# Performance work log

Measured on AMD Instinct MI355X. Metric: run time of the kernel, lower is better.

The kernel has to match this reference:

```python
import jax, jax.numpy as jnp
import numpy as np

NUM_HEADS = 8
HEAD_SPLITS = (2, 3, 3)      # heads per CRPE window (CoaT default {3:2,5:3,7:3})
KERNELS = (3, 5, 7)
DIM = 256
CH = DIM // NUM_HEADS        # 32
N_DET = 100


def setup_inputs() -> dict:
    key = jax.random.key(0)
    ks = jax.random.split(key, 12)
    B, Hs, Ws, C = 4, 128, 128, DIM
    N = Hs * Ws
    inp = {
        "x": jax.random.normal(ks[0], (B, N, C), dtype=jnp.float32),
        "det": jax.random.normal(ks[1], (B, N_DET, C), dtype=jnp.float32),
        "H": Hs,
        "W": Ws,
        # qkv Linear (dim -> 3*dim, bias=True); stored as [in, out] for x @ W
        "qkv_w": jax.random.normal(ks[2], (C, 3 * C), dtype=jnp.float32) * 0.02,
        "qkv_b": jnp.zeros((3 * C,), dtype=jnp.float32),
        # output proj Linear (dim -> dim)
        "proj_w": jax.random.normal(ks[3], (C, C), dtype=jnp.float32) * 0.02,
        "proj_b": jnp.zeros((C,), dtype=jnp.float32),
    }
    # CRPE depthwise conv weights: per window k, channels = head_split * CH
    for i, (hs, k) in enumerate(zip(HEAD_SPLITS, KERNELS)):
        ch = hs * CH
        inp[f"crpe_w{k}"] = jax.random.normal(ks[4 + i], (ch, 1, k, k), dtype=jnp.float32) * 0.05
        inp[f"crpe_b{k}"] = jnp.zeros((ch,), dtype=jnp.float32)
    return inp


def _crpe(q, v, H, W, crpe_w3, crpe_b3, crpe_w5, crpe_b5, crpe_w7, crpe_b7):
    # q, v: [B, h, N, Ch], N == H*W  (CoaT ConvRelPosEnc)
    B, h, N, Ch = q.shape
    v_img = jnp.transpose(v, (0, 1, 3, 2)).reshape(B, h * Ch, H, W)
    splits = np.cumsum([hs * Ch for hs in HEAD_SPLITS])[:-1]
    parts = jnp.split(v_img, splits, axis=1)
    ws = (crpe_w3, crpe_w5, crpe_w7)
    bs = (crpe_b3, crpe_b5, crpe_b7)
    outs = []
    for part, w, b, k in zip(parts, ws, bs, KERNELS):
        pad = k // 2
        o = jax.lax.conv_general_dilated(
            part, w, window_strides=(1, 1), padding=[(pad, pad), (pad, pad)],
            feature_group_count=part.shape[1],  # depthwise
            dimension_numbers=("NCHW", "OIHW", "NCHW"))
        outs.append(o + b[None, :, None, None])
    conv_v = jnp.concatenate(outs, axis=1).reshape(B, h, Ch, N)
    conv_v = jnp.transpose(conv_v, (0, 1, 3, 2))  # [B,h,N,Ch]
    return q * conv_v


def reference(x, det, H, W, qkv_w, qkv_b, proj_w, proj_b,
              crpe_w3, crpe_b3, crpe_w5, crpe_b5, crpe_w7, crpe_b7):
    B, N, C = x.shape
    h = NUM_HEADS
    Ch = C // h
    scale = Ch ** (-0.5)

    xcat = jnp.concatenate([x, det], axis=1)          # [B, N+M, C]
    full_qkv = xcat @ qkv_w + qkv_b                   # [B, N+M, 3C]

    # ---- patch branch: factorized (linear) attention + CRPE ----
    patch_qkv = full_qkv[:, :N, :].reshape(B, N, 3, h, Ch)
    patch_qkv = jnp.transpose(patch_qkv, (2, 0, 3, 1, 4))  # [3,B,h,N,Ch]
    pq, pk, pv = patch_qkv[0], patch_qkv[1], patch_qkv[2]
    k_softmax = jax.nn.softmax(pk, axis=2)                 # softmax over tokens
    factor = jnp.einsum('bhnc,bhnd->bhcd', k_softmax, pv)  # [B,h,Ch,Ch]
    factor_att = jnp.einsum('bhnc,bhcd->bhnd', pq, factor) # [B,h,N,Ch]
    crpe = _crpe(pq, pv, H, W, crpe_w3, crpe_b3, crpe_w5, crpe_b5, crpe_w7, crpe_b7)
    patch_x = scale * factor_att + crpe
    patch_x = jnp.transpose(patch_x, (0, 2, 1, 3)).reshape(B, N, C)

    # ---- det branch: standard softmax self-attention ----
    det_qkv = full_qkv[:, N:, :].reshape(B, -1, 3, h, Ch)
    det_qkv = jnp.transpose(det_qkv, (2, 0, 3, 1, 4))      # [3,B,h,M,Ch]
    dq, dk, dv = det_qkv[0], det_qkv[1], det_qkv[2]
    attn = jax.nn.softmax((dq * scale) @ jnp.swapaxes(dk, -2, -1), axis=-1)
    det_x = jnp.transpose(attn @ dv, (0, 2, 1, 3)).reshape(B, -1, C)

    out = jnp.concatenate([patch_x, det_x], axis=1) @ proj_w + proj_b
    return out[:, :N, :], out[:, N:, :]
```

## Files before the change

### kernel.cpp

```cpp
#include <hip/hip_runtime.h>
#include <hip/hip_fp16.h>

#define NHEADS 8
#define CHD 32
#define CDIM 256
#define C3 768
#define NTOK 16384
#define MDET 100
#define TPB (NTOK + MDET)
#define BATCH 4
#define ROWS (BATCH * TPB)
#define HH 128
#define WW 128
#define SCALE 0.17677669529663687f
#define SCH 32
#define FCH 16

typedef unsigned short u16;
typedef __attribute__((ext_vector_type(8))) __bf16 bf16x8;
typedef __attribute__((ext_vector_type(4))) float f32x4;

__device__ __forceinline__ float bf2f(u16 u) {
  union { unsigned int i; float f; } z; z.i = ((unsigned int)u) << 16; return z.f;
}
__device__ __forceinline__ u16 f2bf(float f) {
  __bf16 h = (__bf16)f;
  return __builtin_bit_cast(unsigned short, h);
}

static const size_t B_QX     = 0;
static const size_t B_KPL    = B_QX + (size_t)ROWS * 256 * 2;
static const size_t B_VPL    = B_KPL + (size_t)ROWS * 256 * 2;
static const size_t B_WQT    = B_VPL + (size_t)ROWS * 256 * 2;
static const size_t B_WPT    = B_WQT + (size_t)768 * 256 * 2;
static const size_t B_PM     = B_WPT + (size_t)256 * 256 * 2;
static const size_t B_PS     = B_PM + 1024 * 32 * 4;
static const size_t B_FPART  = B_PS + 1024 * 32 * 4;
static const size_t B_FACTOR = B_FPART + (size_t)512 * 1024 * 4;
static const size_t B_LSE    = B_FACTOR + 32768 * 4;
static const size_t B_END    = B_LSE + 1024 * 4;

__global__ __launch_bounds__(256)
void wconv(const float* __restrict__ qkv_w, const float* __restrict__ proj_w,
           u16* __restrict__ WqT, u16* __restrict__ WpT) {
  int o = blockIdx.x * 256 + threadIdx.x;
  if (o < 768 * 256) {
    int n = o >> 8, k = o & 255;
    WqT[o] = f2bf(qkv_w[(size_t)k * C3 + n]);
  } else {
    int p = o - 768 * 256;
    int n = p >> 8, k = p & 255;
    WpT[p] = f2bf(proj_w[(size_t)k * CDIM + n]);
  }
}

__global__ __launch_bounds__(256)
void gemm_qkv(const float* __restrict__ x, const float* __restrict__ det,
              const u16* __restrict__ WqT, const float* __restrict__ bias,
              u16* __restrict__ qx, u16* __restrict__ kpl, __half* __restrict__ vpl) {
  const int row0 = blockIdx.x * 128;
  const int col0 = blockIdx.y * 128;
  const int tid = threadIdx.x;
  const int lane = tid & 63;
  const int wid = tid >> 6;
  const int wm = (wid & 1) * 64;
  const int wn = (wid >> 1) * 64;
  const int m16 = lane & 15;
  const int kg8 = (lane >> 4) * 8;

  __shared__ u16 As[128][72];
  __shared__ u16 Bs[128][72];

  const int sr = tid >> 1;
  const int sk = (tid & 1) * 32;

  int grow = row0 + sr;
  int crow = grow < ROWS ? grow : ROWS - 1;
  int bb = crow / TPB, tt = crow - bb * TPB;
  const float* aptr = (tt < NTOK)
      ? x + (size_t)(bb * NTOK + tt) * CDIM
      : det + (size_t)(bb * MDET + (tt - NTOK)) * CDIM;
  const u16* bptr = WqT + (size_t)(col0 + sr) * CDIM;

  f32x4 acc[4][4];
#pragma unroll
  for (int ni = 0; ni < 4; ++ni) {
    float bv = bias[col0 + wn + ni * 16 + m16];
#pragma unroll
    for (int mi = 0; mi < 4; ++mi)
      acc[mi][ni] = (f32x4){bv, bv, bv, bv};
  }

  for (int k0 = 0; k0 < CDIM; k0 += 64) {
#pragma unroll
    for (int j = 0; j < 4; ++j) {
      float4 v0 = *(const float4*)(aptr + k0 + sk + j * 8);
      float4 v1 = *(const float4*)(aptr + k0 + sk + j * 8 + 4);
      ushort4 u0, u1;
      u0.x = f2bf(v0.x); u0.y = f2bf(v0.y); u0.z = f2bf(v0.z); u0.w = f2bf(v0.w);
      u1.x = f2bf(v1.x); u1.y = f2bf(v1.y); u1.z = f2bf(v1.z); u1.w = f2bf(v1.w);
      *(ushort4*)&As[sr][sk + j * 8] = u0;
      *(ushort4*)&As[sr][sk + j * 8 + 4] = u1;
      *(uint4*)&Bs[sr][sk + j * 8] = *(const uint4*)(bptr + k0 + sk + j * 8);
    }
    __syncthreads();
#pragma unroll
    for (int kk = 0; kk < 2; ++kk) {
      bf16x8 af[4], bfr[4];
#pragma unroll
      for (int mi = 0; mi < 4; ++mi)
        af[mi] = *(const bf16x8*)&As[wm + mi * 16 + m16][kk * 32 + kg8];
#pragma unroll
      for (int ni = 0; ni < 4; ++ni)
        bfr[ni] = *(const bf16x8*)&Bs[wn + ni * 16 + m16][kk * 32 + kg8];
#pragma unroll
      for (int mi = 0; mi < 4; ++mi)
#pragma unroll
        for (int ni = 0; ni < 4; ++ni)
          acc[mi][ni] = __builtin_amdgcn_mfma_f32_16x16x32_bf16(
              af[mi], bfr[ni], acc[mi][ni], 0, 0, 0);
    }
    __syncthreads();
  }

  const int rbase = (lane >> 4) * 4;
#pragma unroll
  for (int mi = 0; mi < 4; ++mi) {
#pragma unroll
    for (int r = 0; r < 4; ++r) {
      int rr = row0 + wm + mi * 16 + rbase + r;
      if (rr >= ROWS) continue;
      int b = rr / TPB, t = rr - b * TPB;
#pragma unroll
      for (int ni = 0; ni < 4; ++ni) {
        int col = col0 + wn + ni * 16 + m16;
        float v = acc[mi][ni][r];
        if (col < 256) {
          qx[(size_t)rr * 256 + col] = f2bf(v);
        } else if (col < 512) {
          int cc = col - 256;
          kpl[((size_t)(b * 8 + (cc >> 5)) * TPB + t) * 32 + (cc & 31)] = f2bf(v);
        } else {
          int cc = col - 512;
          vpl[((size_t)(b * 8 + (cc >> 5)) * TPB + t) * 32 + (cc & 31)] = __float2half(v);
        }
      }
    }
  }
}

__global__ __launch_bounds__(256)
void gemm_proj(const u16* __restrict__ xin, const u16* __restrict__ WpT,
               const float* __restrict__ bias, float* __restrict__ dout) {
  const int row0 = blockIdx.x * 128;
  const int col0 = blockIdx.y * 128;
  const int tid = threadIdx.x;
  const int lane = tid & 63;
  const int wid = tid >> 6;
  const int wm = (wid & 1) * 64;
  const int wn = (wid >> 1) * 64;
  const int m16 = lane & 15;
  const int kg8 = (lane >> 4) * 8;

  __shared__ u16 As[128][72];
  __shared__ u16 Bs[128][72];

  const int sr = tid >> 1;
  const int sk = (tid & 1) * 32;

  int grow = row0 + sr;
  int crow = grow < ROWS ? grow : ROWS - 1;
  const u16* aptr = xin + (size_t)crow * CDIM;
  const u16* bptr = WpT + (size_t)(col0 + sr) * CDIM;

  f32x4 acc[4][4];
#pragma unroll
  for (int ni = 0; ni < 4; ++ni) {
    float bv = bias[col0 + wn + ni * 16 + m16];
#pragma unroll
    for (int mi = 0; mi < 4; ++mi)
      acc[mi][ni] = (f32x4){bv, bv, bv, bv};
  }

  for (int k0 = 0; k0 < CDIM; k0 += 64) {
#pragma unroll
    for (int j = 0; j < 4; ++j) {
      *(uint4*)&As[sr][sk + j * 8] = *(const uint4*)(aptr + k0 + sk + j * 8);
      *(uint4*)&Bs[sr][sk + j * 8] = *(const uint4*)(bptr + k0 + sk + j * 8);
    }
    __syncthreads();
#pragma unroll
    for (int kk = 0; kk < 2; ++kk) {
      bf16x8 af[4], bfr[4];
#pragma unroll
      for (int mi = 0; mi < 4; ++mi)
        af[mi] = *(const bf16x8*)&As[wm + mi * 16 + m16][kk * 32 + kg8];
#pragma unroll
      for (int ni = 0; ni < 4; ++ni)
        bfr[ni] = *(const bf16x8*)&Bs[wn + ni * 16 + m16][kk * 32 + kg8];
#pragma unroll
      for (int mi = 0; mi < 4; ++mi)
#pragma unroll
        for (int ni = 0; ni < 4; ++ni)
          acc[mi][ni] = __builtin_amdgcn_mfma_f32_16x16x32_bf16(
              af[mi], bfr[ni], acc[mi][ni], 0, 0, 0);
    }
    __syncthreads();
  }

  const int rbase = (lane >> 4) * 4;
#pragma unroll
  for (int mi = 0; mi < 4; ++mi) {
#pragma unroll
    for (int r = 0; r < 4; ++r) {
      int rr = row0 + wm + mi * 16 + rbase + r;
      if (rr >= ROWS) continue;
      int b = rr / TPB, t = rr - b * TPB;
      float* dst = (t < NTOK)
          ? dout + ((size_t)b * NTOK + t) * CDIM
          : dout + (size_t)BATCH * NTOK * CDIM + ((size_t)b * MDET + (t - NTOK)) * CDIM;
#pragma unroll
      for (int ni = 0; ni < 4; ++ni)
        dst[col0 + wn + ni * 16 + m16] = acc[mi][ni][r];
    }
  }
}

__global__ __launch_bounds__(256)
void kstats(const u16* __restrict__ kpl, float* __restrict__ pm,
            float* __restrict__ ps) {
  const int bid = blockIdx.x;
  const int chunk = bid & (SCH - 1);
  const int h = (bid / SCH) & 7;
  const int b = bid / (SCH * 8);
  const int tid = threadIdx.x;
  const int c = tid & 31, sub = tid >> 5;
  const size_t base = ((size_t)(b * 8 + h) * TPB) * 32 + c;
  const int t0 = chunk * (NTOK / SCH);
  float m = -1e30f, s = 0.f;
  for (int i = sub; i < NTOK / SCH; i += 8) {
    float k = bf2f(kpl[base + (size_t)(t0 + i) * 32]);
    float nm = fmaxf(m, k);
    s = s * __expf(m - nm) + __expf(k - nm);
    m = nm;
  }
  __shared__ float sm[8][32], ss[8][32];
  sm[sub][c] = m; ss[sub][c] = s;
  __syncthreads();
  if (sub == 0) {
    for (int j = 1; j < 8; ++j) {
      float m2 = sm[j][c], s2 = ss[j][c];
      float nm = fmaxf(m, m2);
      s = s * __expf(m - nm) + s2 * __expf(m2 - nm);
      m = nm;
    }
    pm[bid * 32 + c] = m;
    ps[bid * 32 + c] = s;
  }
}

__global__ void kmerge(const float* __restrict__ pm, const float* __restrict__ ps,
                       float* __restrict__ lse) {
  int g = blockIdx.x * blockDim.x + threadIdx.x;
  if (g >= BATCH * 8 * 32) return;
  int c = g & 31, bh = g >> 5;
  float m = -1e30f, s = 0.f;
  for (int ch = 0; ch < SCH; ++ch) {
    int bid = bh * SCH + ch;
    float m2 = pm[bid * 32 + c], s2 = ps[bid * 32 + c];
    float nm = fmaxf(m, m2);
    s = s * __expf(m - nm) + s2 * __expf(m2 - nm);
    m = nm;
  }
  lse[g] = m + logf(s);
}

__global__ __launch_bounds__(256)
void kfactor(const u16* __restrict__ kpl, const __half* __restrict__ vpl,
             const float* __restrict__ lse, float* __restrict__ fpart) {
  const int bid = blockIdx.x;
  const int chunk = bid & (FCH - 1);
  const int h = (bid / FCH) & 7;
  const int b = bid / (FCH * 8);
  const int tid = threadIdx.x;
  const int c = tid & 31;
  const int d0 = (tid >> 5) * 4;
  const float lse_c = lse[(b * 8 + h) * 32 + c];
  __shared__ float wsm[64][32];
  __shared__ float vsm[64][33];
  float a0 = 0.f, a1 = 0.f, a2 = 0.f, a3 = 0.f;
  const int t0 = chunk * (NTOK / FCH);
  for (int st = 0; st < (NTOK / FCH) / 64; ++st) {
    int tb = t0 + st * 64;
    const size_t base = ((size_t)(b * 8 + h) * TPB + tb) * 32;
#pragma unroll
    for (int i = 0; i < 8; ++i) {
      int flat = tid + i * 256;
      int tt = flat >> 5;
      int cc = flat & 31;
      wsm[tt][cc] = __expf(bf2f(kpl[base + flat]) - lse_c);
      vsm[tt][cc] = __half2float(vpl[base + flat]);
    }
    __syncthreads();
#pragma unroll 4
    for (int tt = 0; tt < 64; ++tt) {
      float w = wsm[tt][c];
      a0 += w * vsm[tt][d0 + 0];
      a1 += w * vsm[tt][d0 + 1];
      a2 += w * vsm[tt][d0 + 2];
      a3 += w * vsm[tt][d0 + 3];
    }
    __syncthreads();
  }
  float* fp = fpart + ((size_t)bid * 32 + c) * 32 + d0;
  fp[0] = a0; fp[1] = a1; fp[2] = a2; fp[3] = a3;
}

__global__ void fmerge(const float* __restrict__ fpart, float* __restrict__ factor) {
  int o = blockIdx.x * 256 + threadIdx.x;
  if (o >= BATCH * 8 * CHD * CHD) return;
  int cd = o & 1023, bh = o >> 10;
  float s = 0.f;
  for (int ch = 0; ch < FCH; ++ch)
    s += fpart[((size_t)(bh * FCH + ch) << 10) + cd];
  factor[o] = s;
}

template <int K>
__global__ __launch_bounds__(256)
void kpatch3(const u16* __restrict__ qx, const __half* __restrict__ vpl,
             const float* __restrict__ factor,
             const float* __restrict__ wk, const float* __restrict__ bk,
             int h_base, int nh, u16* __restrict__ xout) {
  constexpr int HE = 16 + K - 1;
  constexpr int PADK = K / 2;
  constexpr int CSTRIDE = HE * 24 + 8;

  __shared__ u16 vt[32 * CSTRIDE];
  __shared__ u16 fa_s[256 * 32];
  __shared__ u16 FT[32 * 32];

  const int bid = blockIdx.x;
  const int tile = bid & 63;
  const int rem = bid >> 6;
  const int h = h_base + (rem % nh);
  const int b = rem / nh;
  const int y0 = (tile >> 3) * 16, x0 = (tile & 7) * 16;
  const int tid = threadIdx.x;
  const int btok = b * TPB;
  const size_t vbase = (size_t)(b * 8 + h) * TPB * 32;

  for (int flat = tid; flat < HE * HE * 8; flat += 256) {
    int pos = flat >> 3, c4 = (flat & 7) * 4;
    int y = pos / HE, xx_ = pos - y * HE;
    int yy = y0 + y - PADK, xx = x0 + xx_ - PADK;
    ushort4 v = make_ushort4(0, 0, 0, 0);
    if (yy >= 0 && yy < HH && xx >= 0 && xx < WW)
      v = *(const ushort4*)((const u16*)vpl + vbase + (size_t)(yy * WW + xx) * 32 + c4);
    vt[(c4 + 0) * CSTRIDE + y * 24 + xx_] = v.x;
    vt[(c4 + 1) * CSTRIDE + y * 24 + xx_] = v.y;
    vt[(c4 + 2) * CSTRIDE + y * 24 + xx_] = v.z;
    vt[(c4 + 3) * CSTRIDE + y * 24 + xx_] = v.w;
  }
  {
    int flat = tid;
    int d = flat >> 5, cc = flat & 31;
    FT[d * 32 + cc] = f2bf(factor[(size_t)((b * 8 + h) << 10) + cc * 32 + d]);
    flat = tid + 256; d = flat >> 5; cc = flat & 31;
    FT[d * 32 + cc] = f2bf(factor[(size_t)((b * 8 + h) << 10) + cc * 32 + d]);
    flat = tid + 512; d = flat >> 5; cc = flat & 31;
    FT[d * 32 + cc] = f2bf(factor[(size_t)((b * 8 + h) << 10) + cc * 32 + d]);
    flat = tid + 768; d = flat >> 5; cc = flat & 31;
    FT[d * 32 + cc] = f2bf(factor[(size_t)((b * 8 + h) << 10) + cc * 32 + d]);
  }
  __syncthreads();

  {
    const int lane = tid & 63;
    const int wid = tid >> 6;
    const int m16 = lane & 15;
    const int kg8 = (lane >> 4) * 8;
    bf16x8 bfr[2];
#pragma unroll
    for (int ni = 0; ni < 2; ++ni)
      bfr[ni] = *(const bf16x8*)&FT[(ni * 16 + m16) * 32 + kg8];
    f32x4 acc[4][2];
#pragma unroll
    for (int mi = 0; mi < 4; ++mi)
#pragma unroll
      for (int ni = 0; ni < 2; ++ni)
        acc[mi][ni] = (f32x4){0.f, 0.f, 0.f, 0.f};
#pragma unroll
    for (int mi = 0; mi < 4; ++mi) {
      int pos = wid * 64 + mi * 16 + m16;
      int token = (y0 + (pos >> 4)) * 128 + x0 + (pos & 15);
      bf16x8 af = *(const bf16x8*)(qx + (size_t)(btok + token) * 256 + h * 32 + kg8);
#pragma unroll
      for (int ni = 0; ni < 2; ++ni)
        acc[mi][ni] = __builtin_amdgcn_mfma_f32_16x16x32_bf16(
            af, bfr[ni], acc[mi][ni], 0, 0, 0);
    }
#pragma unroll
    for (int mi = 0; mi < 4; ++mi)
#pragma unroll
      for (int ni = 0; ni < 2; ++ni)
#pragma unroll
        for (int r = 0; r < 4; ++r) {
          int pos = wid * 64 + mi * 16 + (lane >> 4) * 4 + r;
          fa_s[pos * 32 + ni * 16 + m16] = f2bf(acc[mi][ni][r]);
        }
  }
  __syncthreads();

  const int c = tid & 31;
  const int syg = tid >> 5;
  const int widx = (h - h_base) * 32 + c;
  float wreg[K * K];
#pragma unroll
  for (int i = 0; i < K * K; ++i) wreg[i] = wk[widx * K * K + i];
  const float wb = bk[widx];

  float o[2][16];
#pragma unroll
  for (int ri = 0; ri < 2; ++ri)
#pragma unroll
    for (int p = 0; p < 16; ++p) o[ri][p] = 0.f;

#pragma unroll
  for (int ri = 0; ri < 2; ++ri) {
    const int yy = syg + ri * 8;
#pragma unroll
    for (int dy = 0; dy < K; ++dy) {
      const int vrow = yy + dy;
      union { uint4 q[3]; __half hh[24]; } row;
      row.q[0] = *(const uint4*)&vt[c * CSTRIDE + vrow * 24 + 0];
      row.q[1] = *(const uint4*)&vt[c * CSTRIDE + vrow * 24 + 8];
      row.q[2] = *(const uint4*)&vt[c * CSTRIDE + vrow * 24 + 16];
      float frow[HE];
#pragma unroll
      for (int j = 0; j < HE; ++j) frow[j] = __half2float(row.hh[j]);
#pragma unroll
      for (int dx = 0; dx < K; ++dx) {
        const float wv = wreg[dy * K + dx];
#pragma unroll
        for (int p = 0; p < 16; ++p)
          o[ri][p] += wv * frow[p + dx];
      }
    }
  }

#pragma unroll
  for (int ri = 0; ri < 2; ++ri) {
    const int yy = syg + ri * 8;
#pragma unroll
    for (int p = 0; p < 16; ++p) {
      const int pos = yy * 16 + p;
      const int token = (y0 + yy) * 128 + x0 + p;
      const size_t gidx = (size_t)(btok + token) * 256 + h * 32 + c;
      float fa = bf2f(fa_s[pos * 32 + c]);
      float qv = bf2f(qx[gidx]);
      xout[gidx] = f2bf(SCALE * fa + qv * (o[ri][p] + wb));
    }
  }
}

__global__ __launch_bounds__(128)
void kdet(const u16* __restrict__ qx, const u16* __restrict__ kpl,
          const __half* __restrict__ vpl, u16* __restrict__ xout) {
  const int bid = blockIdx.x;
  const int b = bid >> 3, h = bid & 7;
  const int tid = threadIdx.x;
  __shared__ float qd[100][32], kd[100][32], vd[100][32];
  __shared__ float pd[100][101];
  const size_t rq = ((size_t)b * TPB + NTOK) * CDIM;
  const size_t rp = ((size_t)(b * 8 + h) * TPB + NTOK) * 32;
  for (int flat = tid; flat < 100 * 32; flat += 128) {
    int t = flat >> 5, cc = flat & 31;
    qd[t][cc] = bf2f(qx[rq + (size_t)t * CDIM + h * CHD + cc]);
    kd[t][cc] = bf2f(kpl[rp + (size_t)t * 32 + cc]);
    vd[t][cc] = __half2float(vpl[rp + (size_t)t * 32 + cc]);
  }
  __syncthreads();
  const int r = tid;
  if (r < 100) {
    float mx = -1e30f;
    for (int j = 0; j < 100; ++j) {
      float s = 0.f;
#pragma unroll
      for (int cc = 0; cc < 32; ++cc) s += qd[r][cc] * kd[j][cc];
      s *= SCALE;
      pd[r][j] = s;
      mx = fmaxf(mx, s);
    }
    float sum = 0.f;
    for (int j = 0; j < 100; ++j) {
      float e = __expf(pd[r][j] - mx);
      pd[r][j] = e;
      sum += e;
    }
    float inv = 1.f / sum;
    for (int d = 0; d < 32; ++d) {
      float o = 0.f;
      for (int j = 0; j < 100; ++j) o += pd[r][j] * vd[j][d];
      xout[rq + (size_t)r * CDIM + h * CHD + d] = f2bf(o * inv);
    }
  }
}

extern "C" void kernel_launch(void* const* d_in, const int* in_sizes, int n_in,
                              void* d_out, int out_size, void* d_ws, size_t ws_size,
                              hipStream_t stream) {
  if (ws_size < B_END) return;

  const float* x      = (const float*)d_in[0];
  const float* det    = (const float*)d_in[1];
  const float* qkv_w  = (const float*)d_in[4];
  const float* qkv_b  = (const float*)d_in[5];
  const float* proj_w = (const float*)d_in[6];
  const float* proj_b = (const float*)d_in[7];
  const float* w3     = (const float*)d_in[8];
  const float* b3     = (const float*)d_in[9];
  const float* w5     = (const float*)d_in[10];
  const float* b5     = (const float*)d_in[11];
  const float* w7     = (const float*)d_in[12];
  const float* b7     = (const float*)d_in[13];

  char* wsb = (char*)d_ws;
  u16* qx      = (u16*)(wsb + B_QX);
  u16* kpl     = (u16*)(wsb + B_KPL);
  __half* vpl  = (__half*)(wsb + B_VPL);
  u16* WqT     = (u16*)(wsb + B_WQT);
  u16* WpT     = (u16*)(wsb + B_WPT);
  float* pm    = (float*)(wsb + B_PM);
  float* ps    = (float*)(wsb + B_PS);
  float* fpart = (float*)(wsb + B_FPART);
  float* factor= (float*)(wsb + B_FACTOR);
  float* lse   = (float*)(wsb + B_LSE);
  float* out   = (float*)d_out;

  wconv<<<1024, 256, 0, stream>>>(qkv_w, proj_w, WqT, WpT);

  dim3 g1((ROWS + 127) / 128, C3 / 128);
  gemm_qkv<<<g1, 256, 0, stream>>>(x, det, WqT, qkv_b, qx, kpl, vpl);

  kstats<<<BATCH * 8 * SCH, 256, 0, stream>>>(kpl, pm, ps);
  kmerge<<<4, 256, 0, stream>>>(pm, ps, lse);
  kfactor<<<BATCH * 8 * FCH, 256, 0, stream>>>(kpl, vpl, lse, fpart);
  fmerge<<<128, 256, 0, stream>>>(fpart, factor);

  kpatch3<3><<<BATCH * 2 * 64, 256, 0, stream>>>(qx, vpl, factor, w3, b3, 0, 2, qx);
  kpatch3<5><<<BATCH * 3 * 64, 256, 0, stream>>>(qx, vpl, factor, w5, b5, 2, 3, qx);
  kpatch3<7><<<BATCH * 3 * 64, 256, 0, stream>>>(qx, vpl, factor, w7, b7, 5, 3, qx);

  kdet<<<BATCH * 8, 128, 0, stream>>>(qx, kpl, vpl, qx);

  dim3 g2((ROWS + 127) / 128, CDIM / 128);
  gemm_proj<<<g2, 256, 0, stream>>>(qx, WpT, proj_b, out);
}
```

Before: 442.7 us.

## Pre-convert activations to bf16 in a prep pass and remap QKV GEMM blocks across XCDs

A new prep kernel converts x/det to bf16 once, writing into the output buffer as scratch, and also transposes both weight matrices. The QKV GEMM then loads bf16 A tiles directly instead of re-reading fp32 and converting per column block, which was repeated six times. Its grid becomes 1D, with a remap so that blocks sharing a row tile land on the same XCD for L2 reuse. kfactor also switches to float4 LDS reads of v with no padding and a larger unroll. The cost is an extra full read and write pass over the activations.

```diff
diff --git a/kernel.cpp b/kernel.cpp
--- a/kernel.cpp
+++ b/kernel.cpp
@@ -40,26 +40,63 @@
 static const size_t B_LSE    = B_FACTOR + 32768 * 4;
 static const size_t B_END    = B_LSE + 1024 * 4;
 
+
+#define XCHUNKS (ROWS * 32)
+#define WQCH (768 * 256 / 8)
+#define WPCH (256 * 256 / 8)
+
 __global__ __launch_bounds__(256)
-void wconv(const float* __restrict__ qkv_w, const float* __restrict__ proj_w,
-           u16* __restrict__ WqT, u16* __restrict__ WpT) {
-  int o = blockIdx.x * 256 + threadIdx.x;
-  if (o < 768 * 256) {
-    int n = o >> 8, k = o & 255;
-    WqT[o] = f2bf(qkv_w[(size_t)k * C3 + n]);
-  } else {
-    int p = o - 768 * 256;
-    int n = p >> 8, k = p & 255;
-    WpT[p] = f2bf(proj_w[(size_t)k * CDIM + n]);
+void prep(const float* __restrict__ x, const float* __restrict__ det,
+          const float* __restrict__ qkv_w, const float* __restrict__ proj_w,
+          u16* __restrict__ xbf, u16* __restrict__ WqT, u16* __restrict__ WpT) {
+  const int total = XCHUNKS + WQCH + WPCH;
+  for (int idx = blockIdx.x * 256 + threadIdx.x; idx < total; idx += gridDim.x * 256) {
+    if (idx < XCHUNKS) {
+      int r = idx >> 5;
+      int co = (idx & 31) * 8;
+      int b = r / TPB, t = r - b * TPB;
+      const float* src = (t < NTOK)
+          ? x + (size_t)(b * NTOK + t) * CDIM + co
+          : det + (size_t)(b * MDET + (t - NTOK)) * CDIM + co;
+      float4 v0 = *(const float4*)src;
+      float4 v1 = *(const float4*)(src + 4);
+      ushort4 a, bb;
+      a.x = f2bf(v0.x); a.y = f2bf(v0.y); a.z = f2bf(v0.z); a.w = f2bf(v0.w);
+      bb.x = f2bf(v1.x); bb.y = f2bf(v1.y); bb.z = f2bf(v1.z); bb.w = f2bf(v1.w);
+      *(ushort4*)(xbf + (size_t)idx * 8) = a;
+      *(ushort4*)(xbf + (size_t)idx * 8 + 4) = bb;
+    } else if (idx < XCHUNKS + WQCH) {
+      int o = (idx - XCHUNKS) * 8;
+#pragma unroll
+      for (int j = 0; j < 8; ++j) {
+        int oo = o + j;
+        int n = oo >> 8, k = oo & 255;
+        WqT[oo] = f2bf(qkv_w[(size_t)k * C3 + n]);
+      }
+    } else {
+      int o = (idx - XCHUNKS - WQCH) * 8;
+#pragma unroll
+      for (int j = 0; j < 8; ++j) {
+        int oo = o + j;
+        int n = oo >> 8, k = oo & 255;
+        WpT[oo] = f2bf(proj_w[(size_t)k * CDIM + n]);
+      }
+    }
   }
 }
 
 __global__ __launch_bounds__(256)
-void gemm_qkv(const float* __restrict__ x, const float* __restrict__ det,
-              const u16* __restrict__ WqT, const float* __restrict__ bias,
+void gemm_qkv(const u16* __restrict__ xbf, const u16* __restrict__ WqT,
+              const float* __restrict__ bias,
               u16* __restrict__ qx, u16* __restrict__ kpl, __half* __restrict__ vpl) {
-  const int row0 = blockIdx.x * 128;
-  const int col0 = blockIdx.y * 128;
+  const int bid = blockIdx.x;
+  const int xcd = bid & 7;
+  const int slot = bid >> 3;
+  const int colb = slot % 6;
+  const int rowl = slot / 6;
+  const int row0 = (xcd + 8 * rowl) * 128;
+  const int col0 = colb * 128;
+
   const int tid = threadIdx.x;
   const int lane = tid & 63;
   const int wid = tid >> 6;
@@ -76,10 +113,7 @@
 
   int grow = row0 + sr;
   int crow = grow < ROWS ? grow : ROWS - 1;
-  int bb = crow / TPB, tt = crow - bb * TPB;
-  const float* aptr = (tt < NTOK)
-      ? x + (size_t)(bb * NTOK + tt) * CDIM
-      : det + (size_t)(bb * MDET + (tt - NTOK)) * CDIM;
+  const u16* aptr = xbf + (size_t)crow * CDIM;
   const u16* bptr = WqT + (size_t)(col0 + sr) * CDIM;
 
   f32x4 acc[4][4];
@@ -94,13 +128,7 @@
   for (int k0 = 0; k0 < CDIM; k0 += 64) {
 #pragma unroll
     for (int j = 0; j < 4; ++j) {
-      float4 v0 = *(const float4*)(aptr + k0 + sk + j * 8);
-      float4 v1 = *(const float4*)(aptr + k0 + sk + j * 8 + 4);
-      ushort4 u0, u1;
-      u0.x = f2bf(v0.x); u0.y = f2bf(v0.y); u0.z = f2bf(v0.z); u0.w = f2bf(v0.w);
-      u1.x = f2bf(v1.x); u1.y = f2bf(v1.y); u1.z = f2bf(v1.z); u1.w = f2bf(v1.w);
-      *(ushort4*)&As[sr][sk + j * 8] = u0;
-      *(ushort4*)&As[sr][sk + j * 8 + 4] = u1;
+      *(uint4*)&As[sr][sk + j * 8] = *(const uint4*)(aptr + k0 + sk + j * 8);
       *(uint4*)&Bs[sr][sk + j * 8] = *(const uint4*)(bptr + k0 + sk + j * 8);
     }
     __syncthreads();
@@ -287,7 +315,7 @@
   const int d0 = (tid >> 5) * 4;
   const float lse_c = lse[(b * 8 + h) * 32 + c];
   __shared__ float wsm[64][32];
-  __shared__ float vsm[64][33];
+  __shared__ float vsm[64][32];
   float a0 = 0.f, a1 = 0.f, a2 = 0.f, a3 = 0.f;
   const int t0 = chunk * (NTOK / FCH);
   for (int st = 0; st < (NTOK / FCH) / 64; ++st) {
@@ -302,13 +330,14 @@
       vsm[tt][cc] = __half2float(vpl[base + flat]);
     }
     __syncthreads();
-#pragma unroll 4
+#pragma unroll 8
     for (int tt = 0; tt < 64; ++tt) {
       float w = wsm[tt][c];
-      a0 += w * vsm[tt][d0 + 0];
-      a1 += w * vsm[tt][d0 + 1];
-      a2 += w * vsm[tt][d0 + 2];
-      a3 += w * vsm[tt][d0 + 3];
+      float4 vv = *(const float4*)&vsm[tt][d0];
+      a0 += w * vv.x;
+      a1 += w * vv.y;
+      a2 += w * vv.z;
+      a3 += w * vv.w;
     }
     __syncthreads();
   }
@@ -537,11 +566,11 @@
   float* factor= (float*)(wsb + B_FACTOR);
   float* lse   = (float*)(wsb + B_LSE);
   float* out   = (float*)d_out;
-
-  wconv<<<1024, 256, 0, stream>>>(qkv_w, proj_w, WqT, WpT);
-
-  dim3 g1((ROWS + 127) / 128, C3 / 128);
-  gemm_qkv<<<g1, 256, 0, stream>>>(x, det, WqT, qkv_b, qx, kpl, vpl);
+  u16* xbf     = (u16*)d_out;
+
+  prep<<<4096, 256, 0, stream>>>(x, det, qkv_w, proj_w, xbf, WqT, WpT);
+
+  gemm_qkv<<<3120, 256, 0, stream>>>(xbf, WqT, qkv_b, qx, kpl, vpl);
 
   kstats<<<BATCH * 8 * SCH, 256, 0, stream>>>(kpl, pm, ps);
   kmerge<<<4, 256, 0, stream>>>(pm, ps, lse);
```

Result: faster. 425.4 us (-3.9%).
